# Optimization experiments

Hardware: AMD Instinct MI355X
Metric: run time of the kernel (lower is better)

## Reference

```python
import jax, jax.numpy as jnp
import numpy as np

D_MODEL = 1024
D_INNER = 2048      # expand * d_model
D_STATE = 64
HEADDIM = 128
NHEADS = 16         # d_inner // headdim
D_CONV = 4
CHUNK = 256
D_IN_PROJ = 2 * D_INNER + 2 * D_STATE + NHEADS   # 4240 (ngroups=1)
CONV_DIM = D_INNER + 2 * D_STATE                 # 2176
EPS = 1e-5


def setup_inputs() -> dict:
    key = jax.random.key(0)
    ks = jax.random.split(key, 8)
    B, L = 2, 4096
    u = jax.random.normal(ks[0], (B, L, D_MODEL), jnp.float32)
    in_proj_w = jax.random.normal(ks[1], (D_IN_PROJ, D_MODEL), jnp.float32) / np.sqrt(D_MODEL)
    conv_w = jax.random.uniform(ks[2], (CONV_DIM, D_CONV), jnp.float32, -0.5, 0.5)
    conv_b = jnp.zeros((CONV_DIM,), jnp.float32)
    # dt_bias init exactly as in the module: inv-softplus of dt ~ logU(1e-3, 1e-1)
    dt0 = jnp.exp(jax.random.uniform(ks[3], (NHEADS,), jnp.float32) * (np.log(0.1) - np.log(0.001)) + np.log(0.001))
    dt_bias = dt0 + jnp.log(-jnp.expm1(-dt0))
    A_log = jnp.log(jax.random.uniform(ks[4], (NHEADS,), jnp.float32, 1.0, 16.0))
    Dp = jnp.ones((NHEADS,), jnp.float32)
    norm_w = jnp.ones((D_INNER,), jnp.float32)
    out_proj_w = jax.random.normal(ks[5], (D_MODEL, D_INNER), jnp.float32) / np.sqrt(D_INNER)
    return dict(u=u, in_proj_w=in_proj_w, conv_w=conv_w, conv_b=conv_b, dt_bias=dt_bias,
                A_log=A_log, Dp=Dp, norm_w=norm_w, out_proj_w=out_proj_w)


def _ssd(x, dt, A, Bm, Cm, Dp):
    # Chunked selective state-space scan (mamba_chunk_scan_combined semantics).
    # x: [b,l,h,p], dt: [b,l,h] (already softplus'd), A: [h] (negative), Bm/Cm: [b,l,n]
    b, l, h, p = x.shape
    n = Bm.shape[-1]
    nc = l // CHUNK
    xc = x.reshape(b, nc, CHUNK, h, p)
    dtc = dt.reshape(b, nc, CHUNK, h)
    Bc = Bm.reshape(b, nc, CHUNK, n)
    Cc = Cm.reshape(b, nc, CHUNK, n)
    a = dtc * A                       # [b,c,q,h], a <= 0
    acum = jnp.cumsum(a, axis=2)      # within-chunk cumulative log-decay
    # ---- intra-chunk (causal, attention-like) ----
    scores = jnp.einsum('bcqn,bckn->bcqk', Cc, Bc)
    diff = acum[:, :, :, None, :] - acum[:, :, None, :, :]        # [b,c,q,k,h]
    mask = jnp.tril(jnp.ones((CHUNK, CHUNK), bool))[None, None, :, :, None]
    decay = jnp.exp(jnp.where(mask, diff, -jnp.inf))
    M = scores[..., None] * decay * dtc[:, :, None, :, :]         # [b,c,q,k,h]
    y_diag = jnp.einsum('bcqkh,bckhp->bcqhp', M, xc)
    # ---- per-chunk end states ----
    decay_states = jnp.exp(acum[:, :, -1:, :] - acum)             # [b,c,q,h]
    states = jnp.einsum('bcqh,bcqn,bcqhp->bchpn', dtc * decay_states, Bc, xc)
    # ---- inter-chunk recurrence (scan over nc chunks) ----
    chunk_decay = jnp.exp(acum[:, :, -1, :])                      # [b,c,h]
    def step(s, inp):
        st, cd = inp
        return cd[:, :, None, None] * s + st, s                   # emit state BEFORE this chunk
    init = jnp.zeros((b, h, p, n), x.dtype)
    _, prev = jax.lax.scan(step, init, (states.transpose(1, 0, 2, 3, 4), chunk_decay.transpose(1, 0, 2)))
    prev = prev.transpose(1, 0, 2, 3, 4)                          # [b,c,h,p,n]
    y_off = jnp.einsum('bcqn,bchpn,bcqh->bcqhp', Cc, prev, jnp.exp(acum))
    y = y_diag + y_off + xc * Dp[None, None, None, :, None]
    return y.reshape(b, l, h, p)


def _forward(u, in_proj_w, conv_w, conv_b, dt_bias, A_log, Dp, norm_w, out_proj_w):
    b, l, _ = u.shape
    zxbct = jnp.einsum('bld,ed->ble', u, in_proj_w)
    z = zxbct[..., :D_INNER]
    xBC = zxbct[..., D_INNER:D_INNER + CONV_DIM]
    dt = zxbct[..., D_INNER + CONV_DIM:]
    dt = jax.nn.softplus(dt + dt_bias)                            # [b,l,h]
    # causal depthwise conv1d (padding d_conv-1, truncated to seq_len) + SiLU
    xp = jnp.pad(xBC, ((0, 0), (D_CONV - 1, 0), (0, 0)))
    conv_out = conv_b
    for w in range(D_CONV):
        conv_out = conv_out + xp[:, w:w + l, :] * conv_w[:, w]
    xBC = jax.nn.silu(conv_out)
    x = xBC[..., :D_INNER]
    Bm = xBC[..., D_INNER:D_INNER + D_STATE]
    Cm = xBC[..., D_INNER + D_STATE:]
    A = -jnp.exp(A_log)
    y = _ssd(x.reshape(b, l, NHEADS, HEADDIM), dt, A, Bm, Cm, Dp)
    y = y.reshape(b, l, D_INNER)
    # RMSNormGated (norm_before_gate=False): gate first, then RMSNorm
    y = y * jax.nn.silu(z)
    y = y * jax.lax.rsqrt(jnp.mean(y * y, axis=-1, keepdims=True) + EPS) * norm_w
    return jnp.einsum('ble,de->bld', y, out_proj_w)


def reference(u, in_proj_w, conv_w, conv_b, dt_bias, A_log, Dp, norm_w, out_proj_w):
    return _forward(u, in_proj_w, conv_w, conv_b, dt_bias, A_log, Dp, norm_w, out_proj_w)
```

## Files before the change

### kernel.cpp

```cpp
#include <hip/hip_runtime.h>
#include <hip/hip_bf16.h>
#include <cstdint>
#include <cstddef>

#define D_MODEL   1024
#define D_INNER   2048
#define D_STATE   64
#define HEADDIM   128
#define NHEADS    16
#define D_CONV    4
#define CHUNK     256
#define D_IN_PROJ 4240
#define ZPAD      4352
#define CONV_DIM  2176
#define NB        2
#define LEN       4096
#define NC        16
#define MROWS     (NB*LEN)

typedef __hip_bfloat16 bf16;
typedef __bf16 bf16x8 __attribute__((ext_vector_type(8)));
typedef float  f32x4  __attribute__((ext_vector_type(4)));
typedef unsigned short us4 __attribute__((ext_vector_type(4)));

__device__ __forceinline__ float fsilu(float x){ return x / (1.f + __expf(-x)); }
__device__ __forceinline__ float toF(float x){ return x; }
__device__ __forceinline__ float toF(bf16 x){ return __bfloat162float(x); }
__device__ __forceinline__ void storeF(float* p, float v){ *p = v; }
__device__ __forceinline__ void storeF(bf16* p, float v){ *p = __float2bfloat16(v); }

__device__ __forceinline__ unsigned short f2bs(float v){
  return __bfloat16_as_ushort(__float2bfloat16(v));
}
__device__ __forceinline__ void store4(bf16* p, f32x4 v){
  us4 o; o[0]=f2bs(v[0]); o[1]=f2bs(v[1]); o[2]=f2bs(v[2]); o[3]=f2bs(v[3]);
  *(us4*)p = o;
}
__device__ __forceinline__ void store4(float* p, f32x4 v){
  *(f32x4*)p = v;
}

__device__ __forceinline__ void gload_lds16(const void* g, void* l){
  __builtin_amdgcn_global_load_lds(
     (const __attribute__((address_space(1))) unsigned int*)(uintptr_t)g,
     (__attribute__((address_space(3))) unsigned int*)(uintptr_t)l, 16, 0, 0);
}

template<typename TC>
__global__ __launch_bounds__(256) void k_gemm_mfma(
    const bf16* __restrict__ A, int lda,
    const bf16* __restrict__ B, int ldb,
    TC* __restrict__ C, int ldc, int K)
{
  __shared__ __align__(16) bf16 As[2][128*32];
  __shared__ __align__(16) bf16 Bs[2][128*32];
  const int tid = threadIdx.x;
  const int w = tid >> 6, l = tid & 63;
  const int quad = l >> 4, lq = l & 15;
  const int m0 = blockIdx.x*128, n0 = blockIdx.y*128;
  const int wm = (w & 1)*64, wn = (w >> 1)*64;
  f32x4 acc[4][4] = {};
  const int sr = l >> 2;
  const int sc = (l & 3)*8;

  for (int k0 = 0; k0 < K; k0 += 64) {
    #pragma unroll
    for (int half = 0; half < 2; half++){
      #pragma unroll
      for (int j = 0; j < 2; j++) {
        const int blk = w*2 + j;
        const int row = blk*16 + sr;
        gload_lds16(A + (size_t)(m0+row)*lda + k0 + half*32 + sc, (char*)As[half] + blk*1024);
        gload_lds16(B + (size_t)(n0+row)*ldb + k0 + half*32 + sc, (char*)Bs[half] + blk*1024);
      }
    }
    asm volatile("s_waitcnt vmcnt(0)" ::: "memory");
    __syncthreads();

    const int kq = quad*8;
    #pragma unroll
    for (int half = 0; half < 2; half++){
      bf16x8 af[4], bfr[4];
      #pragma unroll
      for (int t = 0; t < 4; t++){
        af[t]  = *(const bf16x8*)&As[half][(wm + lq + t*16)*32 + kq];
        bfr[t] = *(const bf16x8*)&Bs[half][(wn + lq + t*16)*32 + kq];
      }
      #pragma unroll
      for (int tm = 0; tm < 4; tm++)
        #pragma unroll
        for (int tn = 0; tn < 4; tn++)
          acc[tm][tn] = __builtin_amdgcn_mfma_f32_16x16x32_bf16(bfr[tn], af[tm], acc[tm][tn], 0,0,0);
    }
    __syncthreads();
  }

  #pragma unroll
  for (int tm = 0; tm < 4; tm++){
    int r = m0 + wm + tm*16 + lq;
    #pragma unroll
    for (int tn = 0; tn < 4; tn++){
      int cb = n0 + wn + tn*16 + quad*4;
      store4(&C[(size_t)r*ldc + cb], acc[tm][tn]);
    }
  }
}

#define NU4  (MROWS*D_MODEL/4)
#define NW14 (ZPAD*D_MODEL/4)
#define NW24 (D_MODEL*D_INNER/4)
__global__ __launch_bounds__(256) void k_convert(
    const float* __restrict__ u, const float* __restrict__ Win,
    const float* __restrict__ Wout, const float* __restrict__ norm_w,
    bf16* __restrict__ ub, bf16* __restrict__ Wb_in, bf16* __restrict__ Wb_out){
  int i4 = blockIdx.x*256 + threadIdx.x;
  if (i4 < NU4){
    float4 v = ((const float4*)u)[i4];
    us4 o = {f2bs(v.x), f2bs(v.y), f2bs(v.z), f2bs(v.w)};
    ((us4*)ub)[i4] = o;
  } else if (i4 < NU4 + NW14){
    int j = i4 - NU4;
    int r = j >> 8;
    float4 v = make_float4(0.f,0.f,0.f,0.f);
    if (r < D_IN_PROJ) v = ((const float4*)Win)[j];
    us4 o = {f2bs(v.x), f2bs(v.y), f2bs(v.z), f2bs(v.w)};
    ((us4*)Wb_in)[j] = o;
  } else {
    int j = i4 - NU4 - NW14;
    float4 v = ((const float4*)Wout)[j];
    float4 nw = ((const float4*)norm_w)[j & 511];
    us4 o = {f2bs(v.x*nw.x), f2bs(v.y*nw.y), f2bs(v.z*nw.z), f2bs(v.w*nw.w)};
    ((us4*)Wb_out)[j] = o;
  }
}

__global__ __launch_bounds__(256) void k_dt(
    const bf16* __restrict__ zxbct, const float* __restrict__ dt_bias,
    const float* __restrict__ A_log, float* __restrict__ dt_t,
    float* __restrict__ acum_t, float* __restrict__ cd_t){
  int bid = blockIdx.x;
  int h = bid & 15, c = (bid>>4)&15, b = bid>>8;
  int q = threadIdx.x;
  size_t m = (size_t)(b*NC + c)*CHUNK + q;
  float x = toF(zxbct[m*ZPAD + (D_INNER + CONV_DIM) + h]) + dt_bias[h];
  float dtv = (x > 20.f) ? x : log1pf(__expf(x));
  float Ah = -__expf(A_log[h]);
  float a = dtv * Ah;
  __shared__ float sb[CHUNK];
  sb[q] = a;
  __syncthreads();
  #pragma unroll
  for (int off=1; off<CHUNK; off<<=1){
    float t = (q >= off) ? sb[q-off] : 0.f;
    __syncthreads();
    sb[q] += t;
    __syncthreads();
  }
  float ac = sb[q];
  size_t o = ((size_t)(b*NHEADS+h))*LEN + c*CHUNK + q;
  dt_t[o]   = dtv;
  acum_t[o] = ac;
  if (q == CHUNK-1) cd_t[(b*NHEADS+h)*NC + c] = __expf(ac);
}

__global__ __launch_bounds__(256) void k_conv(
    const bf16* __restrict__ zxbct, const float* __restrict__ conv_w,
    const float* __restrict__ conv_b, bf16* __restrict__ xbc){
  __shared__ __align__(16) __bf16 xs[35*64];
  __shared__ __align__(16) float  ws[64*4];
  __shared__ float bs[64];
  const int tid = threadIdx.x;
  const int cq = tid & 7;
  const int tm = tid >> 3;
  const int c0 = blockIdx.x*64;
  const int m0 = blockIdx.y*32;
  {
    int g = m0 - 3 + tm; if (g < 0) g = 0;
    *(bf16x8*)&xs[tm*64 + cq*8] =
        *(const bf16x8*)(zxbct + (size_t)g*ZPAD + D_INNER + c0 + cq*8);
    if (tid < 24){
      int r2 = 32 + (tid >> 3);
      int g2 = m0 - 3 + r2;
      *(bf16x8*)&xs[r2*64 + cq*8] =
          *(const bf16x8*)(zxbct + (size_t)g2*ZPAD + D_INNER + c0 + cq*8);
    }
  }
  if (tid < 64)      *(float4*)&ws[tid*4] = *(const float4*)(conv_w + (size_t)(c0+tid)*4);
  else if (tid < 128) bs[tid-64] = conv_b[c0 + tid - 64];
  __syncthreads();

  const int m = m0 + tm;
  const int l = m & (LEN-1);
  float acc[8];
  #pragma unroll
  for (int j=0;j<8;j++) acc[j] = bs[cq*8+j];
  #pragma unroll
  for (int w=0; w<D_CONV; w++){
    if (l - (D_CONV-1) + w >= 0){
      bf16x8 v = *(const bf16x8*)&xs[(tm+w)*64 + cq*8];
      #pragma unroll
      for (int j=0;j<8;j++) acc[j] += (float)v[j] * ws[(cq*8+j)*4 + w];
    }
  }
  bf16x8 o;
  #pragma unroll
  for (int j=0;j<8;j++) o[j] = (__bf16)fsilu(acc[j]);
  *(bf16x8*)(xbc + (size_t)m*CONV_DIM + c0 + cq*8) = o;
}

__global__ __launch_bounds__(256,2) void k_fused(
    const bf16* __restrict__ xbc, const float* __restrict__ acum_t,
    const float* __restrict__ dt_t, const float* __restrict__ Dp,
    bf16* __restrict__ y, float* __restrict__ states)
{
  const int bid = blockIdx.x;
  const int h = bid & 15, c = (bid>>4)&15, b = bid>>8;
  const int z = b*NC + c;
  const int tid = threadIdx.x;
  const int w = tid >> 6, l = tid & 63;
  const int quad = l >> 4, lq = l & 15;

  __shared__ __align__(16) __bf16 xsT[128*72];
  __shared__ __align__(16) __bf16 bts[64*72];
  __shared__ __align__(16) __bf16 Ms[4][32*40];
  __shared__ float acs[CHUNK], dts[CHUNK];

  const float* acum = acum_t + ((size_t)(b*NHEADS+h))*LEN + c*CHUNK;
  const float* dtc  = dt_t   + ((size_t)(b*NHEADS+h))*LEN + c*CHUNK;
  const float alast = acum[CHUNK-1];
  acs[tid] = acum[tid];
  dts[tid] = dtc[tid];

  const bf16* xrow = xbc + (size_t)z*CHUNK*CONV_DIM + h*HEADDIM;
  const bf16* Brow = xbc + (size_t)z*CHUNK*CONV_DIM + D_INNER;
  const bf16* Crow = xbc + (size_t)z*CHUNK*CONV_DIM + D_INNER + D_STATE;
  const float Dph = Dp[h];
  const int j0 = w, j1 = 7 - w;

  f32x4 Yacc[2][2][8] = {};
  f32x4 Sst[2][4]  = {};

  for (int t = 0; t < 4; t++){
    const int k0 = t*64;
    __syncthreads();
    {
      const bf16* xr = xrow + (size_t)(k0+l)*CONV_DIM;
      #pragma unroll
      for (int pass=0; pass<4; pass++){
        int pb = w*8 + pass*32;
        bf16x8 v = *(const bf16x8*)(xr + pb);
        #pragma unroll
        for (int j=0;j<8;j++) xsT[(pb+j)*72 + l] = v[j];
      }
      float wl = dts[k0+l] * __expf(alast - acs[k0+l]);
      const bf16* br = Brow + (size_t)(k0+l)*CONV_DIM;
      #pragma unroll
      for (int pass=0; pass<2; pass++){
        int nb = w*8 + pass*32;
        bf16x8 v = *(const bf16x8*)(br + nb);
        #pragma unroll
        for (int j=0;j<8;j++) bts[(nb+j)*72 + l] = (__bf16)((float)v[j] * wl);
      }
    }
    __syncthreads();

    #pragma unroll
    for (int s=0;s<2;s++){
      bf16x8 a2[2];
      #pragma unroll
      for (int mi=0;mi<2;mi++)
        a2[mi] = *(const bf16x8*)&xsT[(w*32 + mi*16 + lq)*72 + s*32 + quad*8];
      #pragma unroll
      for (int ni=0;ni<4;ni++){
        bf16x8 bb = *(const bf16x8*)&bts[(ni*16+lq)*72 + s*32 + quad*8];
        #pragma unroll
        for (int mi=0;mi<2;mi++)
          Sst[mi][ni] = __builtin_amdgcn_mfma_f32_16x16x32_bf16(bb, a2[mi], Sst[mi][ni], 0,0,0);
      }
    }

    #pragma unroll
    for (int half=0; half<2; half++){
      const int j = half ? j1 : j0;
      if (2*t > j) continue;
      const int qbase = j*32;
      bf16x8 cf[2][2];
      #pragma unroll
      for (int s=0;s<2;s++)
        #pragma unroll
        for (int qm=0;qm<2;qm++)
          cf[s][qm] = *(const bf16x8*)(Crow + (size_t)(qbase+qm*16+lq)*CONV_DIM + s*32 + quad*8);
      #pragma unroll
      for (int kk=0; kk<2; kk++){
        const int kh = 2*t + kk;
        if (kh > j) continue;
        const int kb32  = kk*32;
        const int kbase = kh*32;
        f32x4 Sacc[2][2] = {};
        #pragma unroll
        for (int s=0;s<2;s++){
          bf16x8 bfk[2];
          #pragma unroll
          for (int kn=0;kn<2;kn++)
            bfk[kn] = *(const bf16x8*)(Brow + (size_t)(kbase+kn*16+lq)*CONV_DIM + s*32 + quad*8);
          #pragma unroll
          for (int kn=0;kn<2;kn++)
            #pragma unroll
            for (int qm=0;qm<2;qm++)
              Sacc[kn][qm] = __builtin_amdgcn_mfma_f32_16x16x32_bf16(bfk[kn], cf[s][qm], Sacc[kn][qm], 0,0,0);
        }
        #pragma unroll
        for (int qm=0;qm<2;qm++){
          int ql = qbase + qm*16 + lq;
          float aq = acs[ql];
          #pragma unroll
          for (int kn=0;kn<2;kn++){
            us4 o;
            #pragma unroll
            for (int i=0;i<4;i++){
              int kl = kbase + kn*16 + quad*4 + i;
              float v = Sacc[kn][qm][i] * __expf(aq - acs[kl]) * dts[kl];
              v = (kl < ql) ? v : ((kl == ql) ? v + Dph : 0.f);
              o[i] = f2bs(v);
            }
            *(us4*)&Ms[w][(qm*16+lq)*40 + kn*16 + quad*4] = o;
          }
        }
        asm volatile("s_waitcnt lgkmcnt(0)" ::: "memory");
        #pragma unroll
        for (int qm=0;qm<2;qm++){
          bf16x8 am = *(const bf16x8*)&Ms[w][(qm*16+lq)*40 + quad*8];
          #pragma unroll
          for (int pn=0;pn<8;pn++){
            bf16x8 bp = *(const bf16x8*)&xsT[(pn*16+lq)*72 + kb32 + quad*8];
            Yacc[half][qm][pn] = __builtin_amdgcn_mfma_f32_16x16x32_bf16(bp, am, Yacc[half][qm][pn], 0,0,0);
          }
        }
      }
    }
  }

  bf16* yrow = y + (size_t)z*CHUNK*D_INNER + h*HEADDIM;
  #pragma unroll
  for (int half=0; half<2; half++){
    const int j = half ? j1 : j0;
    #pragma unroll
    for (int qm=0;qm<2;qm++){
      int q = j*32 + qm*16 + lq;
      #pragma unroll
      for (int pn=0;pn<8;pn++)
        store4(&yrow[(size_t)q*D_INNER + pn*16 + quad*4], Yacc[half][qm][pn]);
    }
  }
  float* so = states + (size_t)bid*HEADDIM*D_STATE;
  #pragma unroll
  for (int mi=0;mi<2;mi++){
    int pp = w*32 + mi*16 + lq;
    #pragma unroll
    for (int ni=0;ni<4;ni++)
      store4(&so[pp*D_STATE + ni*16 + quad*4], Sst[mi][ni]);
  }
}

__global__ __launch_bounds__(256) void k_scan(
    const float* __restrict__ states, const float* __restrict__ cd_t,
    bf16* __restrict__ prevb){
  int b = blockIdx.x >> 4, h = blockIdx.x & 15;
  int pt = blockIdx.y;
  int tid = threadIdx.x;
  float carry[4] = {0.f,0.f,0.f,0.f};
  for (int c=0;c<NC;c++){
    size_t base = ((size_t)(b*256 + c*16 + h))*HEADDIM*D_STATE + (size_t)pt*1024;
    float cd = cd_t[(b*NHEADS+h)*NC + c];
    #pragma unroll
    for (int i=0;i<4;i++){
      size_t idx = base + (size_t)i*256 + tid;
      prevb[idx] = __float2bfloat16(carry[i]);
      carry[i] = carry[i]*cd + states[idx];
    }
  }
}

__global__ __launch_bounds__(256,2) void k_yoff(
    const bf16* __restrict__ xbc, const bf16* __restrict__ prevb,
    const float* __restrict__ acum_t, bf16* __restrict__ y){
  const int bid = blockIdx.x;
  const int h = bid & 15, c = (bid>>4)&15, b = bid>>8;
  const int z = b*NC + c;
  const int tid = threadIdx.x;
  const int w = tid >> 6, l = tid & 63;
  const int quad = l >> 4, lq = l & 15;
  const bf16* Crow = xbc + (size_t)z*CHUNK*CONV_DIM + D_INNER + D_STATE;
  const bf16* pv = prevb + (size_t)bid*HEADDIM*D_STATE;
  const float* acum = acum_t + ((size_t)(b*NHEADS+h))*LEN + c*CHUNK;
  const int qw = w*64;
  f32x4 acc[4][8] = {};
  #pragma unroll
  for (int s=0;s<2;s++){
    bf16x8 bp[8];
    #pragma unroll
    for (int pn=0;pn<8;pn++)
      bp[pn] = *(const bf16x8*)(pv + (pn*16+lq)*D_STATE + s*32 + quad*8);
    #pragma unroll
    for (int qm=0;qm<4;qm++){
      int row = qw + qm*16 + lq;
      float e = __expf(acum[row]);
      bf16x8 a = *(const bf16x8*)(Crow + (size_t)row*CONV_DIM + s*32 + quad*8);
      bf16x8 ae;
      #pragma unroll
      for (int j=0;j<8;j++) ae[j] = (__bf16)((float)a[j] * e);
      #pragma unroll
      for (int pn=0;pn<8;pn++)
        acc[qm][pn] = __builtin_amdgcn_mfma_f32_16x16x32_bf16(bp[pn], ae, acc[qm][pn], 0,0,0);
    }
  }
  bf16* yrow = y + (size_t)z*CHUNK*D_INNER + h*HEADDIM;
  #pragma unroll
  for (int qm=0;qm<4;qm++){
    int q = qw + qm*16 + lq;
    #pragma unroll
    for (int pn=0;pn<8;pn++){
      bf16* yp = &yrow[(size_t)q*D_INNER + pn*16 + quad*4];
      us4 old = *(const us4*)yp;
      us4 o;
      #pragma unroll
      for (int i=0;i<4;i++)
        o[i] = f2bs(__bfloat162float(__ushort_as_bfloat16(old[i])) + acc[qm][pn][i]);
      *(us4*)yp = o;
    }
  }
}

__global__ __launch_bounds__(256) void k_gatenorm(
    const bf16* __restrict__ zxbct, bf16* __restrict__ y){
  int m = blockIdx.x;
  int e0 = threadIdx.x*8;
  bf16x8 zv = *(const bf16x8*)(zxbct + (size_t)m*ZPAD + e0);
  bf16x8 yv = *(const bf16x8*)(y + (size_t)m*D_INNER + e0);
  float v[8]; float ss = 0.f;
  #pragma unroll
  for (int j=0;j<8;j++){
    float val = (float)yv[j] * fsilu((float)zv[j]);
    v[j] = val; ss += val*val;
  }
  #pragma unroll
  for (int off=32; off>0; off>>=1) ss += __shfl_down(ss, off, 64);
  __shared__ float red[4];
  if ((threadIdx.x & 63) == 0) red[threadIdx.x >> 6] = ss;
  __syncthreads();
  float tot = red[0]+red[1]+red[2]+red[3];
  float r = rsqrtf(tot * (1.f/D_INNER) + 1e-5f);
  bf16x8 o;
  #pragma unroll
  for (int j=0;j<8;j++) o[j] = (__bf16)(v[j] * r);
  *(bf16x8*)(y + (size_t)m*D_INNER + e0) = o;
}

extern "C" void kernel_launch(void* const* d_in, const int* in_sizes, int n_in,
                              void* d_out, int out_size, void* d_ws, size_t ws_size,
                              hipStream_t stream) {
  const float* u         = (const float*)d_in[0];
  const float* in_proj_w = (const float*)d_in[1];
  const float* conv_w    = (const float*)d_in[2];
  const float* conv_b    = (const float*)d_in[3];
  const float* dt_bias   = (const float*)d_in[4];
  const float* A_log     = (const float*)d_in[5];
  const float* Dp        = (const float*)d_in[6];
  const float* norm_w    = (const float*)d_in[7];
  const float* out_proj_w= (const float*)d_in[8];
  float* out = (float*)d_out;

  char* p = (char*)d_ws;
  auto alloc = [&](size_t bytes){ char* r = p; p += (bytes + 255) & ~size_t(255); return r; };
  bf16*  zxbct = (bf16*) alloc((size_t)MROWS*ZPAD*2);
  bf16*  xbc   = (bf16*) alloc((size_t)MROWS*CONV_DIM*2);
  bf16*  y     = (bf16*) alloc((size_t)MROWS*D_INNER*2);
  bf16*  ub    = (bf16*) alloc((size_t)MROWS*D_MODEL*2);
  bf16*  Wb_in = (bf16*) alloc((size_t)ZPAD*D_MODEL*2);
  bf16*  Wb_out= (bf16*) alloc((size_t)D_MODEL*D_INNER*2);
  float* dt_t  = (float*)alloc((size_t)NB*NHEADS*LEN*4);
  float* acum_t= (float*)alloc((size_t)NB*NHEADS*LEN*4);
  float* cd_t  = (float*)alloc((size_t)NB*NHEADS*NC*4);
  float* states= (float*)ub;
  bf16*  prevb = (bf16*)Wb_in;

  dim3 blk(256);
  k_convert<<<dim3((NU4+NW14+NW24)/256), blk, 0, stream>>>(
      u, in_proj_w, out_proj_w, norm_w, ub, Wb_in, Wb_out);

  k_gemm_mfma<bf16><<<dim3(MROWS/128, ZPAD/128), blk, 0, stream>>>(
      ub, D_MODEL, Wb_in, D_MODEL, zxbct, ZPAD, D_MODEL);

  k_dt   <<<dim3(NB*NC*NHEADS), blk, 0, stream>>>(zxbct, dt_bias, A_log, dt_t, acum_t, cd_t);
  k_conv <<<dim3(CONV_DIM/64, MROWS/32), blk, 0, stream>>>(zxbct, conv_w, conv_b, xbc);
  k_fused<<<dim3(NB*NC*NHEADS), blk, 0, stream>>>(xbc, acum_t, dt_t, Dp, y, states);
  k_scan <<<dim3(NB*NHEADS, 8), blk, 0, stream>>>(states, cd_t, prevb);
  k_yoff <<<dim3(NB*NC*NHEADS), blk, 0, stream>>>(xbc, prevb, acum_t, y);
  k_gatenorm<<<dim3(MROWS), blk, 0, stream>>>(zxbct, y);

  k_gemm_mfma<float><<<dim3(MROWS/128, D_MODEL/128), blk, 0, stream>>>(
      y, D_INNER, Wb_out, D_INNER, out, D_MODEL, D_INNER);
}
```

Before: 376.7 us.

## Split chunk-state pass, fuse inter-chunk output into intra kernel, double-buffer staging

Chunk-state computation moves into its own kernel, k_states, which runs before the scan. The intra-chunk kernel now takes the scanned previous states and adds the C·prev contribution straight into its accumulators. This removes the separate k_yoff kernel and its read-modify-write of y in bf16. Both SSD kernels double-buffer the shared-memory staging of x/B tiles, so the next tile's loads overlap the current tile's MFMAs. The conv kernel now processes 64 rows per block instead of 32, which cuts halo reloads. In exchange, x and B are read twice (once in k_states, once in k_fused), and the doubled shared-memory buffers may reduce occupancy.

Measured after the change: 372.9 us. No clear change (-1.0%).

```diff
diff --git a/kernel.cpp b/kernel.cpp
--- a/kernel.cpp
+++ b/kernel.cpp
@@ -166,52 +166,58 @@
 __global__ __launch_bounds__(256) void k_conv(
     const bf16* __restrict__ zxbct, const float* __restrict__ conv_w,
     const float* __restrict__ conv_b, bf16* __restrict__ xbc){
-  __shared__ __align__(16) __bf16 xs[35*64];
+  __shared__ __align__(16) __bf16 xs[67*64];
   __shared__ __align__(16) float  ws[64*4];
   __shared__ float bs[64];
   const int tid = threadIdx.x;
   const int cq = tid & 7;
   const int tm = tid >> 3;
   const int c0 = blockIdx.x*64;
-  const int m0 = blockIdx.y*32;
+  const int m0 = blockIdx.y*64;
   {
     int g = m0 - 3 + tm; if (g < 0) g = 0;
     *(bf16x8*)&xs[tm*64 + cq*8] =
         *(const bf16x8*)(zxbct + (size_t)g*ZPAD + D_INNER + c0 + cq*8);
+    int g2 = m0 - 3 + tm + 32;
+    *(bf16x8*)&xs[(tm+32)*64 + cq*8] =
+        *(const bf16x8*)(zxbct + (size_t)g2*ZPAD + D_INNER + c0 + cq*8);
     if (tid < 24){
-      int r2 = 32 + (tid >> 3);
-      int g2 = m0 - 3 + r2;
-      *(bf16x8*)&xs[r2*64 + cq*8] =
-          *(const bf16x8*)(zxbct + (size_t)g2*ZPAD + D_INNER + c0 + cq*8);
+      int r3 = 64 + (tid >> 3);
+      int g3 = m0 - 3 + r3;
+      *(bf16x8*)&xs[r3*64 + cq*8] =
+          *(const bf16x8*)(zxbct + (size_t)g3*ZPAD + D_INNER + c0 + cq*8);
     }
   }
   if (tid < 64)      *(float4*)&ws[tid*4] = *(const float4*)(conv_w + (size_t)(c0+tid)*4);
   else if (tid < 128) bs[tid-64] = conv_b[c0 + tid - 64];
   __syncthreads();
 
-  const int m = m0 + tm;
-  const int l = m & (LEN-1);
-  float acc[8];
-  #pragma unroll
-  for (int j=0;j<8;j++) acc[j] = bs[cq*8+j];
-  #pragma unroll
-  for (int w=0; w<D_CONV; w++){
-    if (l - (D_CONV-1) + w >= 0){
-      bf16x8 v = *(const bf16x8*)&xs[(tm+w)*64 + cq*8];
-      #pragma unroll
-      for (int j=0;j<8;j++) acc[j] += (float)v[j] * ws[(cq*8+j)*4 + w];
-    }
-  }
-  bf16x8 o;
-  #pragma unroll
-  for (int j=0;j<8;j++) o[j] = (__bf16)fsilu(acc[j]);
-  *(bf16x8*)(xbc + (size_t)m*CONV_DIM + c0 + cq*8) = o;
-}
-
-__global__ __launch_bounds__(256,2) void k_fused(
+  #pragma unroll
+  for (int rr=0; rr<2; rr++){
+    const int r = tm + rr*32;
+    const int m = m0 + r;
+    const int l = m & (LEN-1);
+    float acc[8];
+    #pragma unroll
+    for (int j=0;j<8;j++) acc[j] = bs[cq*8+j];
+    #pragma unroll
+    for (int w=0; w<D_CONV; w++){
+      if (l - (D_CONV-1) + w >= 0){
+        bf16x8 v = *(const bf16x8*)&xs[(r+w)*64 + cq*8];
+        #pragma unroll
+        for (int j=0;j<8;j++) acc[j] += (float)v[j] * ws[(cq*8+j)*4 + w];
+      }
+    }
+    bf16x8 o;
+    #pragma unroll
+    for (int j=0;j<8;j++) o[j] = (__bf16)fsilu(acc[j]);
+    *(bf16x8*)(xbc + (size_t)m*CONV_DIM + c0 + cq*8) = o;
+  }
+}
+
+__global__ __launch_bounds__(256,2) void k_states(
     const bf16* __restrict__ xbc, const float* __restrict__ acum_t,
-    const float* __restrict__ dt_t, const float* __restrict__ Dp,
-    bf16* __restrict__ y, float* __restrict__ states)
+    const float* __restrict__ dt_t, float* __restrict__ states)
 {
   const int bid = blockIdx.x;
   const int h = bid & 15, c = (bid>>4)&15, b = bid>>8;
@@ -220,64 +226,160 @@
   const int w = tid >> 6, l = tid & 63;
   const int quad = l >> 4, lq = l & 15;
 
-  __shared__ __align__(16) __bf16 xsT[128*72];
-  __shared__ __align__(16) __bf16 bts[64*72];
-  __shared__ __align__(16) __bf16 Ms[4][32*40];
-  __shared__ float acs[CHUNK], dts[CHUNK];
+  __shared__ __align__(16) __bf16 xsT[2][128*72];
+  __shared__ __align__(16) __bf16 bts[2][64*72];
 
   const float* acum = acum_t + ((size_t)(b*NHEADS+h))*LEN + c*CHUNK;
   const float* dtc  = dt_t   + ((size_t)(b*NHEADS+h))*LEN + c*CHUNK;
   const float alast = acum[CHUNK-1];
+  const bf16* xrow = xbc + (size_t)z*CHUNK*CONV_DIM + h*HEADDIM;
+  const bf16* Brow = xbc + (size_t)z*CHUNK*CONV_DIM + D_INNER;
+
+  f32x4 Sst[2][4] = {};
+
+  auto stage = [&](int t, int buf){
+    const int k0 = t*64;
+    const bf16* xr = xrow + (size_t)(k0+l)*CONV_DIM;
+    #pragma unroll
+    for (int pass=0; pass<4; pass++){
+      int pb = w*8 + pass*32;
+      bf16x8 v = *(const bf16x8*)(xr + pb);
+      #pragma unroll
+      for (int j=0;j<8;j++) xsT[buf][(pb+j)*72 + l] = v[j];
+    }
+    float wl = dtc[k0+l] * __expf(alast - acum[k0+l]);
+    const bf16* br = Brow + (size_t)(k0+l)*CONV_DIM;
+    #pragma unroll
+    for (int pass=0; pass<2; pass++){
+      int nb = w*8 + pass*32;
+      bf16x8 v = *(const bf16x8*)(br + nb);
+      #pragma unroll
+      for (int j=0;j<8;j++) bts[buf][(nb+j)*72 + l] = (__bf16)((float)v[j] * wl);
+    }
+  };
+
+  stage(0, 0);
+  for (int t = 0; t < 4; t++){
+    const int buf = t & 1;
+    __syncthreads();
+    if (t < 3) stage(t+1, buf^1);
+    #pragma unroll
+    for (int s=0;s<2;s++){
+      bf16x8 a2[2];
+      #pragma unroll
+      for (int mi=0;mi<2;mi++)
+        a2[mi] = *(const bf16x8*)&xsT[buf][(w*32 + mi*16 + lq)*72 + s*32 + quad*8];
+      #pragma unroll
+      for (int ni=0;ni<4;ni++){
+        bf16x8 bb = *(const bf16x8*)&bts[buf][(ni*16+lq)*72 + s*32 + quad*8];
+        #pragma unroll
+        for (int mi=0;mi<2;mi++)
+          Sst[mi][ni] = __builtin_amdgcn_mfma_f32_16x16x32_bf16(bb, a2[mi], Sst[mi][ni], 0,0,0);
+      }
+    }
+  }
+
+  float* so = states + (size_t)bid*HEADDIM*D_STATE;
+  #pragma unroll
+  for (int mi=0;mi<2;mi++){
+    int pp = w*32 + mi*16 + lq;
+    #pragma unroll
+    for (int ni=0;ni<4;ni++)
+      store4(&so[pp*D_STATE + ni*16 + quad*4], Sst[mi][ni]);
+  }
+}
+
+__global__ __launch_bounds__(256) void k_scan(
+    const float* __restrict__ states, const float* __restrict__ cd_t,
+    bf16* __restrict__ prevb){
+  int b = blockIdx.x >> 4, h = blockIdx.x & 15;
+  int pt = blockIdx.y;
+  int tid = threadIdx.x;
+  float carry[4] = {0.f,0.f,0.f,0.f};
+  for (int c=0;c<NC;c++){
+    size_t base = ((size_t)(b*256 + c*16 + h))*HEADDIM*D_STATE + (size_t)pt*1024;
+    float cd = cd_t[(b*NHEADS+h)*NC + c];
+    #pragma unroll
+    for (int i=0;i<4;i++){
+      size_t idx = base + (size_t)i*256 + tid;
+      prevb[idx] = __float2bfloat16(carry[i]);
+      carry[i] = carry[i]*cd + states[idx];
+    }
+  }
+}
+
+__global__ __launch_bounds__(256,2) void k_fused(
+    const bf16* __restrict__ xbc, const float* __restrict__ acum_t,
+    const float* __restrict__ dt_t, const float* __restrict__ Dp,
+    const bf16* __restrict__ prevb, bf16* __restrict__ y)
+{
+  const int bid = blockIdx.x;
+  const int h = bid & 15, c = (bid>>4)&15, b = bid>>8;
+  const int z = b*NC + c;
+  const int tid = threadIdx.x;
+  const int w = tid >> 6, l = tid & 63;
+  const int quad = l >> 4, lq = l & 15;
+
+  __shared__ __align__(16) __bf16 xsT[2][128*72];
+  __shared__ __align__(16) __bf16 Ms[4][32*40];
+  __shared__ float acs[CHUNK], dts[CHUNK];
+
+  const float* acum = acum_t + ((size_t)(b*NHEADS+h))*LEN + c*CHUNK;
+  const float* dtc  = dt_t   + ((size_t)(b*NHEADS+h))*LEN + c*CHUNK;
   acs[tid] = acum[tid];
   dts[tid] = dtc[tid];
 
   const bf16* xrow = xbc + (size_t)z*CHUNK*CONV_DIM + h*HEADDIM;
   const bf16* Brow = xbc + (size_t)z*CHUNK*CONV_DIM + D_INNER;
   const bf16* Crow = xbc + (size_t)z*CHUNK*CONV_DIM + D_INNER + D_STATE;
+  const bf16* pv   = prevb + (size_t)bid*HEADDIM*D_STATE;
   const float Dph = Dp[h];
   const int j0 = w, j1 = 7 - w;
 
   f32x4 Yacc[2][2][8] = {};
-  f32x4 Sst[2][4]  = {};
+
+  auto stage = [&](int t, int buf){
+    const bf16* xr = xrow + (size_t)(t*64+l)*CONV_DIM;
+    #pragma unroll
+    for (int pass=0; pass<4; pass++){
+      int pb = w*8 + pass*32;
+      bf16x8 v = *(const bf16x8*)(xr + pb);
+      #pragma unroll
+      for (int j=0;j<8;j++) xsT[buf][(pb+j)*72 + l] = v[j];
+    }
+  };
+
+  stage(0, 0);
+  __syncthreads();
+
+  #pragma unroll
+  for (int s=0;s<2;s++){
+    bf16x8 bp[8];
+    #pragma unroll
+    for (int pn=0;pn<8;pn++)
+      bp[pn] = *(const bf16x8*)(pv + (pn*16+lq)*D_STATE + s*32 + quad*8);
+    #pragma unroll
+    for (int half=0; half<2; half++){
+      const int j = half ? j1 : j0;
+      #pragma unroll
+      for (int qm=0;qm<2;qm++){
+        int row = j*32 + qm*16 + lq;
+        float e = __expf(acs[row]);
+        bf16x8 a = *(const bf16x8*)(Crow + (size_t)row*CONV_DIM + s*32 + quad*8);
+        bf16x8 ae;
+        #pragma unroll
+        for (int jj=0;jj<8;jj++) ae[jj] = (__bf16)((float)a[jj] * e);
+        #pragma unroll
+        for (int pn=0;pn<8;pn++)
+          Yacc[half][qm][pn] = __builtin_amdgcn_mfma_f32_16x16x32_bf16(bp[pn], ae, Yacc[half][qm][pn], 0,0,0);
+      }
+    }
+  }
 
   for (int t = 0; t < 4; t++){
-    const int k0 = t*64;
-    __syncthreads();
-    {
-      const bf16* xr = xrow + (size_t)(k0+l)*CONV_DIM;
-      #pragma unroll
-      for (int pass=0; pass<4; pass++){
-        int pb = w*8 + pass*32;
-        bf16x8 v = *(const bf16x8*)(xr + pb);
-        #pragma unroll
-        for (int j=0;j<8;j++) xsT[(pb+j)*72 + l] = v[j];
-      }
-      float wl = dts[k0+l] * __expf(alast - acs[k0+l]);
-      const bf16* br = Brow + (size_t)(k0+l)*CONV_DIM;
-      #pragma unroll
-      for (int pass=0; pass<2; pass++){
-        int nb = w*8 + pass*32;
-        bf16x8 v = *(const bf16x8*)(br + nb);
-        #pragma unroll
-        for (int j=0;j<8;j++) bts[(nb+j)*72 + l] = (__bf16)((float)v[j] * wl);
-      }
-    }
-    __syncthreads();
-
-    #pragma unroll
-    for (int s=0;s<2;s++){
-      bf16x8 a2[2];
-      #pragma unroll
-      for (int mi=0;mi<2;mi++)
-        a2[mi] = *(const bf16x8*)&xsT[(w*32 + mi*16 + lq)*72 + s*32 + quad*8];
-      #pragma unroll
-      for (int ni=0;ni<4;ni++){
-        bf16x8 bb = *(const bf16x8*)&bts[(ni*16+lq)*72 + s*32 + quad*8];
-        #pragma unroll
-        for (int mi=0;mi<2;mi++)
-          Sst[mi][ni] = __builtin_amdgcn_mfma_f32_16x16x32_bf16(bb, a2[mi], Sst[mi][ni], 0,0,0);
-      }
-    }
+    const int buf = t & 1;
+    if (t > 0) __syncthreads();
+    if (t < 3) stage(t+1, buf^1);
 
     #pragma unroll
     for (int half=0; half<2; half++){
@@ -332,7 +434,7 @@
           bf16x8 am = *(const bf16x8*)&Ms[w][(qm*16+lq)*40 + quad*8];
           #pragma unroll
           for (int pn=0;pn<8;pn++){
-            bf16x8 bp = *(const bf16x8*)&xsT[(pn*16+lq)*72 + kb32 + quad*8];
+            bf16x8 bp = *(const bf16x8*)&xsT[buf][(pn*16+lq)*72 + kb32 + quad*8];
             Yacc[half][qm][pn] = __builtin_amdgcn_mfma_f32_16x16x32_bf16(bp, am, Yacc[half][qm][pn], 0,0,0);
           }
         }
@@ -350,83 +452,6 @@
       #pragma unroll
       for (int pn=0;pn<8;pn++)
         store4(&yrow[(size_t)q*D_INNER + pn*16 + quad*4], Yacc[half][qm][pn]);
-    }
-  }
-  float* so = states + (size_t)bid*HEADDIM*D_STATE;
-  #pragma unroll
-  for (int mi=0;mi<2;mi++){
-    int pp = w*32 + mi*16 + lq;
-    #pragma unroll
-    for (int ni=0;ni<4;ni++)
-      store4(&so[pp*D_STATE + ni*16 + quad*4], Sst[mi][ni]);
-  }
-}
-
-__global__ __launch_bounds__(256) void k_scan(
-    const float* __restrict__ states, const float* __restrict__ cd_t,
-    bf16* __restrict__ prevb){
-  int b = blockIdx.x >> 4, h = blockIdx.x & 15;
-  int pt = blockIdx.y;
-  int tid = threadIdx.x;
-  float carry[4] = {0.f,0.f,0.f,0.f};
-  for (int c=0;c<NC;c++){
-    size_t base = ((size_t)(b*256 + c*16 + h))*HEADDIM*D_STATE + (size_t)pt*1024;
-    float cd = cd_t[(b*NHEADS+h)*NC + c];
-    #pragma unroll
-    for (int i=0;i<4;i++){
-      size_t idx = base + (size_t)i*256 + tid;
-      prevb[idx] = __float2bfloat16(carry[i]);
-      carry[i] = carry[i]*cd + states[idx];
-    }
-  }
-}
-
-__global__ __launch_bounds__(256,2) void k_yoff(
-    const bf16* __restrict__ xbc, const bf16* __restrict__ prevb,
-    const float* __restrict__ acum_t, bf16* __restrict__ y){
-  const int bid = blockIdx.x;
-  const int h = bid & 15, c = (bid>>4)&15, b = bid>>8;
-  const int z = b*NC + c;
-  const int tid = threadIdx.x;
-  const int w = tid >> 6, l = tid & 63;
-  const int quad = l >> 4, lq = l & 15;
-  const bf16* Crow = xbc + (size_t)z*CHUNK*CONV_DIM + D_INNER + D_STATE;
-  const bf16* pv = prevb + (size_t)bid*HEADDIM*D_STATE;
-  const float* acum = acum_t + ((size_t)(b*NHEADS+h))*LEN + c*CHUNK;
-  const int qw = w*64;
-  f32x4 acc[4][8] = {};
-  #pragma unroll
-  for (int s=0;s<2;s++){
-    bf16x8 bp[8];
-    #pragma unroll
-    for (int pn=0;pn<8;pn++)
-      bp[pn] = *(const bf16x8*)(pv + (pn*16+lq)*D_STATE + s*32 + quad*8);
-    #pragma unroll
-    for (int qm=0;qm<4;qm++){
-      int row = qw + qm*16 + lq;
-      float e = __expf(acum[row]);
-      bf16x8 a = *(const bf16x8*)(Crow + (size_t)row*CONV_DIM + s*32 + quad*8);
-      bf16x8 ae;
-      #pragma unroll
-      for (int j=0;j<8;j++) ae[j] = (__bf16)((float)a[j] * e);
-      #pragma unroll
-      for (int pn=0;pn<8;pn++)
-        acc[qm][pn] = __builtin_amdgcn_mfma_f32_16x16x32_bf16(bp[pn], ae, acc[qm][pn], 0,0,0);
-    }
-  }
-  bf16* yrow = y + (size_t)z*CHUNK*D_INNER + h*HEADDIM;
-  #pragma unroll
-  for (int qm=0;qm<4;qm++){
-    int q = qw + qm*16 + lq;
-    #pragma unroll
-    for (int pn=0;pn<8;pn++){
-      bf16* yp = &yrow[(size_t)q*D_INNER + pn*16 + quad*4];
-      us4 old = *(const us4*)yp;
-      us4 o;
-      #pragma unroll
-      for (int i=0;i<4;i++)
-        o[i] = f2bs(__bfloat162float(__ushort_as_bfloat16(old[i])) + acc[qm][pn][i]);
-      *(us4*)yp = o;
     }
   }
 }
@@ -491,11 +516,11 @@
   k_gemm_mfma<bf16><<<dim3(MROWS/128, ZPAD/128), blk, 0, stream>>>(
       ub, D_MODEL, Wb_in, D_MODEL, zxbct, ZPAD, D_MODEL);
 
-  k_dt   <<<dim3(NB*NC*NHEADS), blk, 0, stream>>>(zxbct, dt_bias, A_log, dt_t, acum_t, cd_t);
-  k_conv <<<dim3(CONV_DIM/64, MROWS/32), blk, 0, stream>>>(zxbct, conv_w, conv_b, xbc);
-  k_fused<<<dim3(NB*NC*NHEADS), blk, 0, stream>>>(xbc, acum_t, dt_t, Dp, y, states);
-  k_scan <<<dim3(NB*NHEADS, 8), blk, 0, stream>>>(states, cd_t, prevb);
-  k_yoff <<<dim3(NB*NC*NHEADS), blk, 0, stream>>>(xbc, prevb, acum_t, y);
+  k_dt    <<<dim3(NB*NC*NHEADS), blk, 0, stream>>>(zxbct, dt_bias, A_log, dt_t, acum_t, cd_t);
+  k_conv  <<<dim3(CONV_DIM/64, MROWS/64), blk, 0, stream>>>(zxbct, conv_w, conv_b, xbc);
+  k_states<<<dim3(NB*NC*NHEADS), blk, 0, stream>>>(xbc, acum_t, dt_t, states);
+  k_scan  <<<dim3(NB*NHEADS, 8), blk, 0, stream>>>(states, cd_t, prevb);
+  k_fused <<<dim3(NB*NC*NHEADS), blk, 0, stream>>>(xbc, acum_t, dt_t, Dp, prevb, y);
   k_gatenorm<<<dim3(MROWS), blk, 0, stream>>>(zxbct, y);
 
   k_gemm_mfma<float><<<dim3(MROWS/128, D_MODEL/128), blk, 0, stream>>>(
```
